# Kernel optimization log

Hardware: AMD Instinct MI355X
Metric: run time of the kernel (lower is better)

The kernel has to match this reference:

```python
import jax, jax.numpy as jnp
import numpy as np
import math

B, S, E = 2, 2048, 1024
H = 16
D = E // H  # head dim = 64


def setup_inputs() -> dict:
    key = jax.random.key(0)
    ks = jax.random.split(key, 9)
    s = 1.0 / math.sqrt(E)
    return {
        "x": jax.random.normal(ks[0], (B, S, E), dtype=jnp.float32),
        "Wq": jax.random.uniform(ks[1], (E, E), jnp.float32, -s, s),
        "bq": jnp.zeros((E,), jnp.float32),
        "Wk": jax.random.uniform(ks[2], (E, E), jnp.float32, -s, s),
        "bk": jnp.zeros((E,), jnp.float32),
        "Wv": jax.random.uniform(ks[3], (E, E), jnp.float32, -s, s),
        "bv": jnp.zeros((E,), jnp.float32),
        "Wo": jax.random.uniform(ks[4], (E, E), jnp.float32, -s, s),
        "bo": jnp.zeros((E,), jnp.float32),
    }


def reference(x, Wq, bq, Wk, bk, Wv, bv, Wo, bo):
    b, s, e = x.shape
    q = x @ Wq + bq  # [B,S,E]
    k = x @ Wk + bk
    v = x @ Wv + bv
    # [B,S,E] -> [B,H,S,D]
    q = q.reshape(b, s, H, D).transpose(0, 2, 1, 3)
    k = k.reshape(b, s, H, D).transpose(0, 2, 1, 3)
    v = v.reshape(b, s, H, D).transpose(0, 2, 1, 3)
    scores = jnp.einsum('bhqd,bhkd->bhqk', q, k) / jnp.sqrt(jnp.float32(D))
    causal = jnp.tril(jnp.ones((s, s), dtype=bool))  # keep lower triangle
    scores = jnp.where(causal, scores, -jnp.inf)
    attn = jax.nn.softmax(scores, axis=-1)
    # dropout is identity in eval mode
    out = jnp.einsum('bhqk,bhkd->bhqd', attn, v)
    out = out.transpose(0, 2, 1, 3).reshape(b, s, e)
    return out @ Wo + bo
```

## Files before the change

### kernel.cpp

```cpp
#include <hip/hip_runtime.h>
#include <hip/hip_bf16.h>
#include <math.h>

#define B_ 2
#define S_ 2048
#define E_ 1024
#define H_ 16
#define D_ 64
#define M_ (B_*S_)

typedef __attribute__((ext_vector_type(8))) short short8v;
typedef __attribute__((ext_vector_type(4))) float floatx4;

__device__ __forceinline__ short f2bf(float f) {
    union { float f; unsigned u; } x; x.f = f;
    unsigned r = (x.u + 0x7fffu + ((x.u >> 16) & 1u)) >> 16;
    return (short)r;
}

__device__ __forceinline__ unsigned pk_bf16(float a, float b) {
    union { float f; unsigned u; } x, y;
    x.f = a; y.f = b;
    return __builtin_amdgcn_perm(y.u + 0x8000u, x.u + 0x8000u, 0x07060302u);
}

__device__ __forceinline__ float fast_exp2(float x) {
#if __has_builtin(__builtin_amdgcn_exp2f)
    return __builtin_amdgcn_exp2f(x);
#else
    return __expf(x * 0.6931471805599453f);
#endif
}

__device__ __forceinline__ void gl2lds16(const void* g, void* l) {
    __builtin_amdgcn_global_load_lds(
        (const __attribute__((address_space(1))) void*)g,
        (__attribute__((address_space(3))) void*)l, 16, 0, 0);
}

__device__ __forceinline__ int swz_off(int row, int cg) {
    return row*64 + (((cg ^ (row & 7)) & 7) << 3);
}

__global__ __launch_bounds__(256) void convert_x(
    const float* __restrict__ x, short* __restrict__ xb)
{
    const size_t i = ((size_t)blockIdx.x*256 + threadIdx.x) * 8;
    float4 a = *(const float4*)(x + i);
    float4 b = *(const float4*)(x + i + 4);
    int4 p = { (int)pk_bf16(a.x,a.y), (int)pk_bf16(a.z,a.w),
               (int)pk_bf16(b.x,b.y), (int)pk_bf16(b.z,b.w) };
    *(int4*)(xb + i) = p;
}

__global__ __launch_bounds__(256) void transpose_w(
    const float* __restrict__ W0, const float* __restrict__ W1,
    const float* __restrict__ W2, const float* __restrict__ W3,
    short* __restrict__ T0, short* __restrict__ T1,
    short* __restrict__ T2, short* __restrict__ T3)
{
    const int z = blockIdx.z;
    const float* W = (z==0)?W0:(z==1)?W1:(z==2)?W2:W3;
    short*       T = (z==0)?T0:(z==1)?T1:(z==2)?T2:T3;
    __shared__ float tile[32][33];
    const int k0 = blockIdx.y*32, n0 = blockIdx.x*32;
    const int r = threadIdx.x >> 5, c = threadIdx.x & 31;
    #pragma unroll
    for (int i=0;i<4;i++)
        tile[r+8*i][c] = W[(size_t)(k0+r+8*i)*E_ + n0 + c];
    __syncthreads();
    #pragma unroll
    for (int i=0;i<4;i++)
        T[(size_t)(n0+r+8*i)*E_ + k0 + c] = f2bf(tile[c][r+8*i]);
}

__global__ __launch_bounds__(256) void qkv_gemm(
    const short* __restrict__ xb, const short* __restrict__ Wt,
    const float* __restrict__ bq, const float* __restrict__ bk, const float* __restrict__ bv,
    short* __restrict__ Qo, short* __restrict__ Ko, short* __restrict__ Vo)
{
    __shared__ __align__(16) short As[128*64];
    __shared__ __align__(16) short Bs[128*64];

    const int t = threadIdx.x;
    const int wave = t >> 6, lane = t & 63;
    const int quad = lane >> 4, l15 = lane & 15;
    const int lin = blockIdx.x;
    const int m0  = (lin & 31) * 128;
    const int nf0 = (lin >> 5) * 128;
    const int z   = nf0 >> 10;
    const float* bb = (z==0) ? bq : (z==1) ? bk : bv;
    short* out      = (z==0) ? Qo : (z==1) ? Ko : Vo;
    const float sc  = (z==0) ? 0.18033688011112042f : 1.0f;

    const int mq = (wave & 1)*64, nq = (wave >> 1)*64;
    const int sr8 = lane >> 3;
    const int scs = ((lane & 7) ^ sr8) * 8;

    floatx4 acc[4][4];
    #pragma unroll
    for (int i=0;i<4;i++)
        #pragma unroll
        for (int j=0;j<4;j++) acc[i][j] = (floatx4){0.f,0.f,0.f,0.f};

    for (int k0 = 0; k0 < E_; k0 += 64) {
        #pragma unroll
        for (int c=0;c<4;c++) {
            const int rb = wave*32 + c*8;
            gl2lds16(xb + (size_t)(m0 +rb+sr8)*E_ + k0 + scs, &As[rb*64]);
            gl2lds16(Wt + (size_t)(nf0+rb+sr8)*E_ + k0 + scs, &Bs[rb*64]);
        }
        __syncthreads();
        #pragma unroll
        for (int ks=0; ks<2; ks++) {
            const int cg = quad + ks*4;
            short8v a[4], b[4];
            #pragma unroll
            for (int mt=0;mt<4;mt++) a[mt] = *(const short8v*)&As[swz_off(mq+mt*16+l15, cg)];
            #pragma unroll
            for (int nt=0;nt<4;nt++) b[nt] = *(const short8v*)&Bs[swz_off(nq+nt*16+l15, cg)];
            #pragma unroll
            for (int mt=0;mt<4;mt++)
                #pragma unroll
                for (int nt=0;nt<4;nt++)
                    acc[mt][nt] = __builtin_amdgcn_mfma_f32_16x16x32_bf16(a[mt], b[nt], acc[mt][nt], 0,0,0);
        }
        __syncthreads();
    }

    #pragma unroll
    for (int nt=0;nt<4;nt++) {
        const int nw = (nf0 & 1023) + nq + nt*16 + l15;
        const float bias = bb[nw];
        const int h = nw >> 6, d = nw & 63;
        #pragma unroll
        for (int mt=0;mt<4;mt++) {
            #pragma unroll
            for (int r=0;r<4;r++) {
                const int m = m0 + mq + mt*16 + quad*4 + r;
                const int b2 = m >> 11, s = m & (S_-1);
                const int bh = (b2<<4) + h;
                const float v = (acc[mt][nt][r] + bias) * sc;
                if (z == 0) {
                    out[((size_t)bh*S_ + s)*D_ + d] = f2bf(v);
                } else if (z == 1) {
                    const int ts = s >> 6, kk = s & 63;
                    const int c = kk*8 + ((d>>3) ^ ((kk>>2)&7));
                    out[((size_t)bh*32 + ts)*4096 + c*8 + (d&7)] = f2bf(v);
                } else {
                    const int ts = s >> 6, sk = s & 63;
                    const int c = d*8 + ((sk>>3) ^ (d&7));
                    out[((size_t)bh*32 + ts)*4096 + c*8 + (sk&7)] = f2bf(v);
                }
            }
        }
    }
}

__global__ __launch_bounds__(256, 1) void attn_kernel(
    const short* __restrict__ Q, const short* __restrict__ K, const short* __restrict__ V,
    short* __restrict__ AO)
{
    const int bh = blockIdx.x;
    const int qb = (gridDim.y - 1 - blockIdx.y) * 128;
    const int t = threadIdx.x;
    const int wave = t >> 6, lane = t & 63;
    const int quad = lane >> 4, l15 = lane & 15;

    const short* Qp = Q + (size_t)bh * (S_*D_);
    const short* Kp = K + (size_t)bh * (S_*D_);
    const short* Vp = V + (size_t)bh * (S_*D_);

    __shared__ __align__(16) short KVs[2][8192];
    __shared__ __align__(16) short Psl[2][4][2][16*72];

    const int qA = qb + wave*16;
    const int qB = qb + 64 + wave*16;
    const short* qa = Qp + (size_t)(qA + l15)*D_ + quad*8;
    const short8v qA0 = *(const short8v*)qa, qA1 = *(const short8v*)(qa + 32);
    const short* qbp = Qp + (size_t)(qB + l15)*D_ + quad*8;
    const short8v qB0 = *(const short8v*)qbp, qB1 = *(const short8v*)(qbp + 32);

    const int qrbA = qA + quad*4;
    const int qrbB = qB + quad*4;

    floatx4 oA[4], oB[4];
    #pragma unroll
    for (int i=0;i<4;i++) { oA[i] = (floatx4){0,0,0,0}; oB[i] = (floatx4){0,0,0,0}; }
    float tsA[4] = {0,0,0,0}, tsB[4] = {0,0,0,0};

    const int L = (qb >> 6) + 2;
    const int swz = l15 & 7;

    auto stage = [&](int kt, int p) {
        const short* src = ((wave < 2) ? Kp : Vp) + (size_t)kt*4096 + (wave&1)*2048 + lane*8;
        short* dst = &KVs[p][((wave < 2) ? 0 : 4096) + (wave&1)*2048];
        #pragma unroll
        for (int c=0;c<4;c++)
            gl2lds16(src + c*512, dst + c*512);
    };
    auto qk2 = [&](const short* KL, floatx4 (&sA)[4], floatx4 (&sB)[4]) {
        #pragma unroll
        for (int h=0; h<4; h++) {
            const int rowc = (4*l15 + h)*8;
            short8v b0 = *(const short8v*)(KL + (rowc + (quad       ^ swz))*8);
            short8v b1 = *(const short8v*)(KL + (rowc + ((4 + quad) ^ swz))*8);
            sA[h] = (floatx4){0.f,0.f,0.f,0.f};
            sA[h] = __builtin_amdgcn_mfma_f32_16x16x32_bf16(qA0, b0, sA[h], 0,0,0);
            sA[h] = __builtin_amdgcn_mfma_f32_16x16x32_bf16(qA1, b1, sA[h], 0,0,0);
            sB[h] = (floatx4){0.f,0.f,0.f,0.f};
            sB[h] = __builtin_amdgcn_mfma_f32_16x16x32_bf16(qB0, b0, sB[h], 0,0,0);
            sB[h] = __builtin_amdgcn_mfma_f32_16x16x32_bf16(qB1, b1, sB[h], 0,0,0);
        }
    };
    auto soft_u = [&](floatx4 (&s)[4], float* ts, short* pw, int qrb, int k0) {
        const int kk = k0 + 4*l15;
        #pragma unroll
        for (int r=0; r<4; r++) {
            const int qr = qrb + r;
            float p[4];
            #pragma unroll
            for (int h=0; h<4; h++) {
                const float e = fast_exp2(s[h][r]);
                p[h] = (kk + h > qr) ? 0.f : e;
            }
            ts[r] += (p[0] + p[1]) + (p[2] + p[3]);
            int2 pkv = { (int)pk_bf16(p[0], p[1]), (int)pk_bf16(p[2], p[3]) };
            *(int2*)(pw + (quad*4 + r)*72 + l15*4) = pkv;
        }
    };
    short8v vr[4][2];
    auto loadv = [&](const short* VL) {
        #pragma unroll
        for (int dt=0; dt<4; dt++) {
            const int rowc = (dt*16 + l15)*8;
            vr[dt][0] = *(const short8v*)(VL + (rowc + (quad       ^ swz))*8);
            vr[dt][1] = *(const short8v*)(VL + (rowc + ((4 + quad) ^ swz))*8);
        }
    };
    auto pv = [&](const short* pw, floatx4 (&o)[4]) {
        const short8v pf0 = *(const short8v*)(pw + l15*72 + quad*8);
        const short8v pf1 = *(const short8v*)(pw + l15*72 + 32 + quad*8);
        #pragma unroll
        for (int dt=0; dt<4; dt++) {
            o[dt] = __builtin_amdgcn_mfma_f32_16x16x32_bf16(pf0, vr[dt][0], o[dt], 0,0,0);
            o[dt] = __builtin_amdgcn_mfma_f32_16x16x32_bf16(pf1, vr[dt][1], o[dt], 0,0,0);
        }
    };

    stage(0, 0);
    __syncthreads();
    stage(1, 1);
    {
        floatx4 sA[4], sB[4];
        qk2(&KVs[0][0], sA, sB);
        loadv(&KVs[0][4096]);
        soft_u(sA, tsA, &Psl[0][wave][0][0], qrbA, 0);
        soft_u(sB, tsB, &Psl[0][wave][1][0], qrbB, 0);
    }

    for (int kt = 1; kt < L; kt++) {
        const int p = kt & 1;
        __syncthreads();
        if (kt + 1 < L) stage(kt + 1, p ^ 1);
        floatx4 sA[4], sB[4];
        qk2(&KVs[p][0], sA, sB);
        pv(&Psl[p^1][wave][0][0], oA);
        pv(&Psl[p^1][wave][1][0], oB);
        loadv(&KVs[p][4096]);
        const int k0 = kt << 6;
        soft_u(sA, tsA, &Psl[p][wave][0][0], qrbA, k0);
        soft_u(sB, tsB, &Psl[p][wave][1][0], qrbB, k0);
    }

    pv(&Psl[1][wave][0][0], oA);
    pv(&Psl[1][wave][1][0], oB);

    float lA[4], lB[4];
    #pragma unroll
    for (int r=0; r<4; r++) {
        float a = tsA[r], b = tsB[r];
        #pragma unroll
        for (int off=1; off<16; off<<=1) {
            a += __shfl_xor(a, off);
            b += __shfl_xor(b, off);
        }
        lA[r] = a; lB[r] = b;
    }

    const int b = bh >> 4, h = bh & 15;
    #pragma unroll
    for (int dt=0; dt<4; dt++) {
        #pragma unroll
        for (int r=0; r<4; r++) {
            const int d = dt*16 + l15;
            const int sA_ = qA + quad*4 + r;
            const int sB_ = qB + quad*4 + r;
            AO[((size_t)(b*S_ + sA_)*H_ + h)*D_ + d] = f2bf(oA[dt][r] / lA[r]);
            AO[((size_t)(b*S_ + sB_)*H_ + h)*D_ + d] = f2bf(oB[dt][r] / lB[r]);
        }
    }
}

__global__ __launch_bounds__(256) void out_gemm(
    const short* __restrict__ A, const short* __restrict__ Wto,
    const float* __restrict__ bo, float* __restrict__ out)
{
    __shared__ __align__(16) short As[128*64];
    __shared__ __align__(16) short Bs[64*64];

    const int t = threadIdx.x;
    const int wave = t >> 6, lane = t & 63;
    const int quad = lane >> 4, l15 = lane & 15;
    const int lin = blockIdx.x;
    const int m0 = (lin & 31) * 128;
    const int n0 = (lin >> 5) * 64;
    const int sr8 = lane >> 3;
    const int scs = ((lane & 7) ^ sr8) * 8;

    floatx4 acc[2][4];
    #pragma unroll
    for (int i=0;i<2;i++)
        #pragma unroll
        for (int j=0;j<4;j++) acc[i][j] = (floatx4){0.f,0.f,0.f,0.f};

    for (int k0 = 0; k0 < E_; k0 += 64) {
        #pragma unroll
        for (int c=0;c<4;c++) {
            const int rb = wave*32 + c*8;
            gl2lds16(A + (size_t)(m0+rb+sr8)*E_ + k0 + scs, &As[rb*64]);
        }
        #pragma unroll
        for (int c=0;c<2;c++) {
            const int rb = wave*16 + c*8;
            gl2lds16(Wto + (size_t)(n0+rb+sr8)*E_ + k0 + scs, &Bs[rb*64]);
        }
        __syncthreads();
        #pragma unroll
        for (int ks=0; ks<2; ks++) {
            const int cg = quad + ks*4;
            short8v a[2], b[4];
            #pragma unroll
            for (int mt=0;mt<2;mt++) a[mt] = *(const short8v*)&As[swz_off(wave*32+mt*16+l15, cg)];
            #pragma unroll
            for (int nt=0;nt<4;nt++) b[nt] = *(const short8v*)&Bs[swz_off(nt*16+l15, cg)];
            #pragma unroll
            for (int mt=0;mt<2;mt++)
                #pragma unroll
                for (int nt=0;nt<4;nt++)
                    acc[mt][nt] = __builtin_amdgcn_mfma_f32_16x16x32_bf16(a[mt], b[nt], acc[mt][nt], 0,0,0);
        }
        __syncthreads();
    }

    #pragma unroll
    for (int nt=0;nt<4;nt++) {
        const int n = n0 + nt*16 + l15;
        const float bias = bo[n];
        #pragma unroll
        for (int mt=0;mt<2;mt++) {
            #pragma unroll
            for (int r=0;r<4;r++) {
                const int m = m0 + wave*32 + mt*16 + quad*4 + r;
                out[(size_t)m*E_ + n] = acc[mt][nt][r] + bias;
            }
        }
    }
}

extern "C" void kernel_launch(void* const* d_in, const int* in_sizes, int n_in,
                              void* d_out, int out_size, void* d_ws, size_t ws_size,
                              hipStream_t stream)
{
    const float* x  = (const float*)d_in[0];
    const float* Wq = (const float*)d_in[1];
    const float* bq = (const float*)d_in[2];
    const float* Wk = (const float*)d_in[3];
    const float* bk = (const float*)d_in[4];
    const float* Wv = (const float*)d_in[5];
    const float* bv = (const float*)d_in[6];
    const float* Wo = (const float*)d_in[7];
    const float* bo = (const float*)d_in[8];

    short* xb  = (short*)d_ws;
    short* Tq  = xb  + (size_t)M_ * E_;
    short* Tk  = Tq  + (size_t)E_ * E_;
    short* Tv  = Tk  + (size_t)E_ * E_;
    short* To  = Tv  + (size_t)E_ * E_;
    short* Qw  = To  + (size_t)E_ * E_;
    short* Kw  = Qw  + (size_t)M_ * E_;
    short* Vw  = Kw  + (size_t)M_ * E_;
    short* AOw = Vw  + (size_t)M_ * E_;

    dim3 blk(256);
    convert_x<<<dim3((M_*E_)/(256*8)), blk, 0, stream>>>(x, xb);
    transpose_w<<<dim3(E_/32, E_/32, 4), blk, 0, stream>>>(Wq, Wk, Wv, Wo, Tq, Tk, Tv, To);
    qkv_gemm<<<dim3(768), blk, 0, stream>>>(xb, Tq, bq, bk, bv, Qw, Kw, Vw);
    attn_kernel<<<dim3(B_*H_, S_/128), blk, 0, stream>>>(Qw, Kw, Vw, AOw);
    out_gemm<<<dim3(512), blk, 0, stream>>>(AOw, To, bo, (float*)d_out);
}
```

Before: 196.8 us.

## Restructure QKV GEMM into 256x256 double-buffered, 8-wave pipelined tiles

Rewrites the QKV projection GEMM to use 256x256 output tiles with 512 threads (8 waves) and double-buffered LDS. Global-to-LDS loads for the next k-tiles are interleaved with MFMA phases, using explicit barriers, s_setprio and vmcnt waits. A swizzled block-index mapping is added to improve L2 reuse. The goal is to hide memory latency and raise arithmetic intensity. In exchange the kernel uses 128KB of LDS and launches only 192 blocks, which may underfill the CUs and lowers occupancy.

```diff
diff --git a/kernel.cpp b/kernel.cpp
--- a/kernel.cpp
+++ b/kernel.cpp
@@ -74,70 +74,132 @@
         T[(size_t)(n0+r+8*i)*E_ + k0 + c] = f2bf(tile[c][r+8*i]);
 }
 
-__global__ __launch_bounds__(256) void qkv_gemm(
+__global__ __launch_bounds__(512, 2) void qkv_gemm(
     const short* __restrict__ xb, const short* __restrict__ Wt,
     const float* __restrict__ bq, const float* __restrict__ bk, const float* __restrict__ bv,
     short* __restrict__ Qo, short* __restrict__ Ko, short* __restrict__ Vo)
 {
-    __shared__ __align__(16) short As[128*64];
-    __shared__ __align__(16) short Bs[128*64];
+    __shared__ __align__(16) short As[2][256*64];
+    __shared__ __align__(16) short Bs[2][256*64];
 
     const int t = threadIdx.x;
     const int wave = t >> 6, lane = t & 63;
     const int quad = lane >> 4, l15 = lane & 15;
-    const int lin = blockIdx.x;
-    const int m0  = (lin & 31) * 128;
-    const int nf0 = (lin >> 5) * 128;
+    const int wr = wave >> 2, wc = wave & 3;
+
+    const int bid = blockIdx.x;
+    const int sw  = (bid & 7) * 24 + (bid >> 3);
+    const int m0  = (sw / 12) * 256;
+    const int nti = sw % 12;
+    const int nf0 = nti * 256;
     const int z   = nf0 >> 10;
     const float* bb = (z==0) ? bq : (z==1) ? bk : bv;
     short* out      = (z==0) ? Qo : (z==1) ? Ko : Vo;
     const float sc  = (z==0) ? 0.18033688011112042f : 1.0f;
 
-    const int mq = (wave & 1)*64, nq = (wave >> 1)*64;
     const int sr8 = lane >> 3;
     const int scs = ((lane & 7) ^ sr8) * 8;
 
-    floatx4 acc[4][4];
-    #pragma unroll
-    for (int i=0;i<4;i++)
+    const short* Ag = xb + (size_t)m0  * E_;
+    const short* Bg = Wt + (size_t)nf0 * E_;
+
+    floatx4 acc[8][4];
+    #pragma unroll
+    for (int i=0;i<8;i++)
         #pragma unroll
         for (int j=0;j<4;j++) acc[i][j] = (floatx4){0.f,0.f,0.f,0.f};
 
-    for (int k0 = 0; k0 < E_; k0 += 64) {
-        #pragma unroll
-        for (int c=0;c<4;c++) {
-            const int rb = wave*32 + c*8;
-            gl2lds16(xb + (size_t)(m0 +rb+sr8)*E_ + k0 + scs, &As[rb*64]);
-            gl2lds16(Wt + (size_t)(nf0+rb+sr8)*E_ + k0 + scs, &Bs[rb*64]);
-        }
-        __syncthreads();
-        #pragma unroll
-        for (int ks=0; ks<2; ks++) {
-            const int cg = quad + ks*4;
-            short8v a[4], b[4];
-            #pragma unroll
-            for (int mt=0;mt<4;mt++) a[mt] = *(const short8v*)&As[swz_off(mq+mt*16+l15, cg)];
-            #pragma unroll
-            for (int nt=0;nt<4;nt++) b[nt] = *(const short8v*)&Bs[swz_off(nq+nt*16+l15, cg)];
-            #pragma unroll
-            for (int mt=0;mt<4;mt++)
+    auto stageA = [&](int p, int h, int kt) {
+        const int rb = h*128 + wave*16;
+        const short* src = Ag + (size_t)(rb + sr8)*E_ + kt*64 + scs;
+        #pragma unroll
+        for (int c=0;c<2;c++)
+            gl2lds16(src + (size_t)c*8*E_, &As[p][(rb + c*8)*64]);
+    };
+    auto stageB = [&](int p, int h, int kt) {
+        const int rb = h*128 + wave*16;
+        const short* src = Bg + (size_t)(rb + sr8)*E_ + kt*64 + scs;
+        #pragma unroll
+        for (int c=0;c<2;c++)
+            gl2lds16(src + (size_t)c*8*E_, &Bs[p][(rb + c*8)*64]);
+    };
+
+    short8v a[4][2], b[4][2];
+    auto rdA = [&](int p, int row16, int ks) -> short8v {
+        return *(const short8v*)&As[p][swz_off(wr*128 + row16*16 + l15, quad + ks*4)];
+    };
+    auto rdB = [&](int p, int row16, int ks) -> short8v {
+        return *(const short8v*)&Bs[p][swz_off(wc*64  + row16*16 + l15, quad + ks*4)];
+    };
+    auto mm = [&](int mbase, int nbase) {
+        #pragma unroll
+        for (int mt=0;mt<4;mt++)
+            #pragma unroll
+            for (int nt=0;nt<2;nt++)
                 #pragma unroll
-                for (int nt=0;nt<4;nt++)
-                    acc[mt][nt] = __builtin_amdgcn_mfma_f32_16x16x32_bf16(a[mt], b[nt], acc[mt][nt], 0,0,0);
-        }
-        __syncthreads();
+                for (int ks=0;ks<2;ks++)
+                    acc[mbase+mt][nbase+nt] = __builtin_amdgcn_mfma_f32_16x16x32_bf16(
+                        a[mt][ks], b[nbase+nt][ks], acc[mbase+mt][nbase+nt], 0,0,0);
+    };
+
+    auto ktile = [&](int tt, int p) {
+        #pragma unroll
+        for (int mt=0;mt<4;mt++){ a[mt][0]=rdA(p,mt,0); a[mt][1]=rdA(p,mt,1); }
+        #pragma unroll
+        for (int nt=0;nt<2;nt++){ b[nt][0]=rdB(p,nt,0); b[nt][1]=rdB(p,nt,1); }
+        if (tt+1 < 16) stageA(p^1, 0, tt+1);
+        __builtin_amdgcn_s_barrier();
+        __builtin_amdgcn_s_setprio(1);
+        mm(0,0);
+        __builtin_amdgcn_s_setprio(0);
+        __builtin_amdgcn_s_barrier();
+        #pragma unroll
+        for (int nt=2;nt<4;nt++){ b[nt][0]=rdB(p,nt,0); b[nt][1]=rdB(p,nt,1); }
+        if (tt+1 < 16) stageA(p^1, 1, tt+1);
+        __builtin_amdgcn_s_barrier();
+        __builtin_amdgcn_s_setprio(1);
+        mm(0,2);
+        __builtin_amdgcn_s_setprio(0);
+        __builtin_amdgcn_s_barrier();
+        #pragma unroll
+        for (int mt=0;mt<4;mt++){ a[mt][0]=rdA(p,4+mt,0); a[mt][1]=rdA(p,4+mt,1); }
+        if (tt+2 < 16) stageB(p, 0, tt+2);
+        __builtin_amdgcn_s_barrier();
+        __builtin_amdgcn_s_setprio(1);
+        mm(4,0);
+        __builtin_amdgcn_s_setprio(0);
+        __builtin_amdgcn_s_barrier();
+        if (tt+2 < 16) stageB(p, 1, tt+2);
+        __builtin_amdgcn_s_barrier();
+        __builtin_amdgcn_s_setprio(1);
+        mm(4,2);
+        __builtin_amdgcn_s_setprio(0);
+        if (tt+2 < 16)      asm volatile("s_waitcnt vmcnt(4)" ::: "memory");
+        else if (tt+1 < 16) asm volatile("s_waitcnt vmcnt(0)" ::: "memory");
+        __builtin_amdgcn_s_barrier();
+    };
+
+    stageA(0,0,0); stageA(0,1,0); stageB(0,0,0); stageB(0,1,0);
+    stageB(1,0,1); stageB(1,1,1);
+    asm volatile("s_waitcnt vmcnt(4)" ::: "memory");
+    __builtin_amdgcn_s_barrier();
+
+    #pragma unroll 1
+    for (int tb = 0; tb < 16; tb += 2) {
+        ktile(tb,   0);
+        ktile(tb+1, 1);
     }
 
     #pragma unroll
     for (int nt=0;nt<4;nt++) {
-        const int nw = (nf0 & 1023) + nq + nt*16 + l15;
+        const int nw = (nf0 & 1023) + wc*64 + nt*16 + l15;
         const float bias = bb[nw];
         const int h = nw >> 6, d = nw & 63;
         #pragma unroll
-        for (int mt=0;mt<4;mt++) {
+        for (int mt=0;mt<8;mt++) {
             #pragma unroll
             for (int r=0;r<4;r++) {
-                const int m = m0 + mq + mt*16 + quad*4 + r;
+                const int m = m0 + wr*128 + mt*16 + quad*4 + r;
                 const int b2 = m >> 11, s = m & (S_-1);
                 const int bh = (b2<<4) + h;
                 const float v = (acc[mt][nt][r] + bias) * sc;
@@ -395,7 +457,7 @@
     dim3 blk(256);
     convert_x<<<dim3((M_*E_)/(256*8)), blk, 0, stream>>>(x, xb);
     transpose_w<<<dim3(E_/32, E_/32, 4), blk, 0, stream>>>(Wq, Wk, Wv, Wo, Tq, Tk, Tv, To);
-    qkv_gemm<<<dim3(768), blk, 0, stream>>>(xb, Tq, bq, bk, bv, Qw, Kw, Vw);
+    qkv_gemm<<<dim3(192), dim3(512), 0, stream>>>(xb, Tq, bq, bk, bv, Qw, Kw, Vw);
     attn_kernel<<<dim3(B_*H_, S_/128), blk, 0, stream>>>(Qw, Kw, Vw, AOw);
     out_gemm<<<dim3(512), blk, 0, stream>>>(AOw, To, bo, (float*)d_out);
 }
```

Measured after the change: 195.5 us. Within noise of the previous version (-0.7%).
